# Performance work log

Measured on AMD Instinct MI355X. Metric: run time of the kernel, lower is better.

The kernel has to match this reference:

```python
import jax, jax.numpy as jnp
import numpy as np

HIDDEN = 4096
NH = 32        # num attention heads
NKV = 8        # num key/value heads
HD = 128       # q/k head dim
VHD = 96       # v head dim
ROT = 64       # rotary dim = int(HD * 0.5)
THETA = 10000.0
B, S = 2, 2048


def setup_inputs() -> dict:
    key = jax.random.key(0)
    ks = jax.random.split(key, 6)
    w = 0.02
    return {
        "hidden_states": jax.random.normal(ks[0], (B, S, HIDDEN), jnp.float32),
        "position_ids": jnp.arange(B * S, dtype=jnp.int32).reshape(B, S) % S,
        "Wq": jax.random.normal(ks[1], (NH * HD, HIDDEN), jnp.float32) * w,
        "Wk": jax.random.normal(ks[2], (NKV * HD, HIDDEN), jnp.float32) * w,
        "Wv": jax.random.normal(ks[3], (NKV * VHD, HIDDEN), jnp.float32) * w,
        "Wo": jax.random.normal(ks[4], (HIDDEN, NH * VHD), jnp.float32) * w,
    }


def _rotate_half(x):
    x1, x2 = x[..., : x.shape[-1] // 2], x[..., x.shape[-1] // 2 :]
    return jnp.concatenate((-x2, x1), axis=-1)


def reference(hidden_states, position_ids, Wq, Wk, Wv, Wo):
    b, s, _ = hidden_states.shape
    # QKV projections (torch Linear: y = x @ W^T)
    q = (hidden_states @ Wq.T).reshape(b, s, NH, HD).transpose(0, 2, 1, 3)   # [b,NH,s,HD]
    k = (hidden_states @ Wk.T).reshape(b, s, NKV, HD).transpose(0, 2, 1, 3)  # [b,NKV,s,HD]
    v = (hidden_states @ Wv.T).reshape(b, s, NKV, VHD).transpose(0, 2, 1, 3)  # [b,NKV,s,VHD]

    # rotary embedding over first ROT dims (partial RoPE)
    inv_freq = 1.0 / (THETA ** (jnp.arange(0, ROT, 2, dtype=jnp.float32) / ROT))  # [ROT/2]
    freqs = position_ids.astype(jnp.float32)[:, :, None] * inv_freq              # [b,s,ROT/2]
    emb = jnp.concatenate((freqs, freqs), axis=-1)                                # [b,s,ROT]
    cos = jnp.cos(emb)[:, None, :, :].astype(hidden_states.dtype)                 # [b,1,s,ROT]
    sin = jnp.sin(emb)[:, None, :, :].astype(hidden_states.dtype)

    q_rot, q_pass = q[..., :ROT], q[..., ROT:]
    k_rot, k_pass = k[..., :ROT], k[..., ROT:]
    q_rot = q_rot * cos + _rotate_half(q_rot) * sin
    k_rot = k_rot * cos + _rotate_half(k_rot) * sin
    q = jnp.concatenate((q_rot, q_pass), axis=-1)
    k = jnp.concatenate((k_rot, k_pass), axis=-1)

    # GQA: repeat_kv (repeat_interleave over head dim)
    n_rep = NH // NKV
    k = jnp.repeat(k, n_rep, axis=1)  # [b,NH,s,HD]
    v = jnp.repeat(v, n_rep, axis=1)  # [b,NH,s,VHD]

    scores = jnp.einsum("bhqd,bhkd->bhqk", q, k) / np.float32(np.sqrt(HD))
    # causal additive mask (attention_mask as built by the HF model)
    neg = jnp.finfo(jnp.float32).min
    causal = jnp.where(jnp.tril(jnp.ones((s, s), dtype=bool)), 0.0, neg)
    scores = scores + causal[None, None, :, :]

    attn = jax.nn.softmax(scores.astype(jnp.float32), axis=-1).astype(q.dtype)
    out = jnp.einsum("bhqk,bhkd->bhqd", attn, v)          # [b,NH,s,VHD]
    out = out.transpose(0, 2, 1, 3).reshape(b, s, NH * VHD)
    return out @ Wo.T                                      # [b,s,HIDDEN]
```

## Files before the change

kernel.cpp:

```cpp
#include <hip/hip_runtime.h>

typedef __attribute__((ext_vector_type(4))) float f32x4;
typedef __attribute__((ext_vector_type(8))) __bf16 bf16x8;
typedef __attribute__((ext_vector_type(8))) unsigned short u16x8;
typedef __attribute__((ext_vector_type(4))) unsigned short u16x4;
typedef __attribute__((ext_vector_type(4))) short s16x4;
typedef unsigned short ushort_t;

__device__ __forceinline__ unsigned short f2bf(float x) {
  unsigned u = __builtin_bit_cast(unsigned, x);
  u += 0x7fffu + ((u >> 16) & 1u);
  return (unsigned short)(u >> 16);
}
__device__ __forceinline__ float bf2f(unsigned short h) {
  unsigned u = ((unsigned)h) << 16;
  return __builtin_bit_cast(float, u);
}
__device__ __forceinline__ short f2bf_n(float x) {
  return __builtin_bit_cast(short, (__bf16)x);
}

__device__ __forceinline__ void gload_lds16(const void* g, void* l) {
  __builtin_amdgcn_global_load_lds(
      (const __attribute__((address_space(1))) unsigned int*)g,
      (__attribute__((address_space(3))) unsigned int*)l, 16, 0, 0);
}

__global__ __launch_bounds__(256) void k_f32_to_bf16(
    const float* __restrict__ src, ushort_t* __restrict__ dst, int n8) {
  int i = blockIdx.x * 256 + threadIdx.x;
  if (i >= n8) return;
  float4 a = ((const float4*)src)[i * 2 + 0];
  float4 b = ((const float4*)src)[i * 2 + 1];
  u16x8 o;
  o[0] = f2bf(a.x); o[1] = f2bf(a.y); o[2] = f2bf(a.z); o[3] = f2bf(a.w);
  o[4] = f2bf(b.x); o[5] = f2bf(b.y); o[6] = f2bf(b.z); o[7] = f2bf(b.w);
  ((u16x8*)dst)[i] = o;
}

__global__ __launch_bounds__(256) void k_rope(
    ushort_t* __restrict__ QKV, const int* __restrict__ pos_ids) {
  int idx = blockIdx.x * 256 + threadIdx.x;
  if (idx >= 4096 * 40 * 32) return;
  int d = idx & 31;
  int rem = idx >> 5;
  int hh = rem % 40;
  int tk = rem / 40;
  int pos = pos_ids[tk];
  float inv = exp2f(-(float)d * (13.287712379549449f / 32.0f));
  float ang = (float)pos * inv;
  float s, c;
  __sincosf(ang, &s, &c);
  int col = (hh < 32) ? (hh * 128 + d) : (4096 + (hh - 32) * 128 + d);
  ushort_t* p = QKV + (size_t)tk * 5888 + col;
  float x1 = bf2f(p[0]);
  float x2 = bf2f(p[32]);
  p[0]  = f2bf(x1 * c - x2 * s);
  p[32] = f2bf(x2 * c + x1 * s);
}

template <int OUT_BF16>
__global__ __launch_bounds__(256, 2) void k_gemm_bt(
    const ushort_t* __restrict__ A, const ushort_t* __restrict__ B,
    void* __restrict__ C, int K, int lda, int ldb, int ldc) {
  __shared__ ushort_t lA[128 * 64];
  __shared__ ushort_t lB[128 * 64];
  const int t = threadIdx.x;
  const int ln = t & 63, w = t >> 6;
  const int fr = ln & 15, fg = ln >> 4;
  const int m0 = blockIdx.x * 128, n0 = blockIdx.y * 128;
  const int wr = (w >> 1) * 64, wc = (w & 1) * 64;

  const int srow = t >> 3;
  const int scol = ((((t & 7) * 16) ^ ((srow & 7) << 4)) >> 1);
  const ushort_t* pA = A + (srow + m0) * lda + scol;
  const ushort_t* pB = B + (srow + n0) * ldb + scol;
  char* lAb = (char*)lA + (w << 10);
  char* lBb = (char*)lB + (w << 10);

  f32x4 acc[4][4] = {};

  for (int k0 = 0; k0 < K; k0 += 64) {
    __syncthreads();
#pragma unroll
    for (int i = 0; i < 4; ++i) {
      gload_lds16(pA + i * 32 * lda + k0, lAb + i * 4096);
      gload_lds16(pB + i * 32 * ldb + k0, lBb + i * 4096);
    }
    __syncthreads();
#pragma unroll
    for (int kh = 0; kh < 2; ++kh) {
      bf16x8 af[4], bfv[4];
#pragma unroll
      for (int m = 0; m < 4; ++m) {
        int row = wr + m * 16 + fr;
        af[m] = *(const bf16x8*)((const char*)lA + row * 128 +
                                 ((kh * 64 + fg * 16) ^ ((row & 7) << 4)));
      }
#pragma unroll
      for (int n = 0; n < 4; ++n) {
        int row = wc + n * 16 + fr;
        bfv[n] = *(const bf16x8*)((const char*)lB + row * 128 +
                                  ((kh * 64 + fg * 16) ^ ((row & 7) << 4)));
      }
#pragma unroll
      for (int m = 0; m < 4; ++m)
#pragma unroll
        for (int n = 0; n < 4; ++n)
          acc[m][n] = __builtin_amdgcn_mfma_f32_16x16x32_bf16(
              af[m], bfv[n], acc[m][n], 0, 0, 0);
    }
  }
#pragma unroll
  for (int m = 0; m < 4; ++m)
#pragma unroll
    for (int n = 0; n < 4; ++n) {
      int row = m0 + wr + m * 16 + fg * 4;
      int col = n0 + wc + n * 16 + fr;
#pragma unroll
      for (int j = 0; j < 4; ++j) {
        if (OUT_BF16)
          ((ushort_t*)C)[(size_t)(row + j) * ldc + col] = f2bf(acc[m][n][j]);
        else
          ((float*)C)[(size_t)(row + j) * ldc + col] = acc[m][n][j];
      }
    }
}

__global__ __launch_bounds__(256, 2) void k_attn(
    const ushort_t* __restrict__ QKV, ushort_t* __restrict__ O) {
  __shared__ ushort_t lK[64 * 128];
  __shared__ ushort_t lV[16 * 96 * 4];

  const int t = threadIdx.x, ln = t & 63, w = t >> 6;
  const int fr = ln & 15, fg = ln >> 4;
  const int h = blockIdx.y, b = blockIdx.z;
  const int qt = ((h >> 4) & 1) ? (15 - (int)blockIdx.x) : (int)blockIdx.x;
  const int hk = h >> 2;
  const int q0 = qt * 128 + w * 32;
  const int tb = b * 2048;

  bf16x8 qf[2][4];
#pragma unroll
  for (int rq = 0; rq < 2; ++rq)
#pragma unroll
    for (int kb = 0; kb < 4; ++kb)
      qf[rq][kb] = *(const bf16x8*)(QKV +
                    (size_t)(tb + q0 + rq * 16 + fr) * 5888 + h * 128 +
                    kb * 32 + fg * 8);

  f32x4 oacc[6][2] = {};
  float mreg[2] = {-1e30f, -1e30f};
  float lreg[2] = {0.f, 0.f};

  const int krow = t >> 4;
  const int kse = ((((t & 15) * 16) ^ (((t >> 4) & 7) << 4)) >> 1);
  const int k4s = t / 12, c8s = t % 12;

  const float sc = 0.088388347648318447f;
  const float l2e = 1.4426950408889634f;
  const float scl2e = sc * l2e;

  const int nkt = (qt + 1) * 2;
  for (int kt = 0; kt < nkt; ++kt) {
    const int kb0 = kt * 64;
    __syncthreads();
    {
      const ushort_t* pK =
          QKV + (size_t)(tb + kb0 + krow) * 5888 + 4096 + hk * 128 + kse;
#pragma unroll
      for (int i = 0; i < 4; ++i)
        gload_lds16(pK + (size_t)i * 16 * 5888,
                    (char*)lK + i * 4096 + (w << 10));
    }
    if (t < 192) {
      const ushort_t* pV =
          QKV + (size_t)(tb + kb0 + k4s * 4) * 5888 + 5120 + hk * 96 + c8s * 8;
      u16x8 vrow[4];
#pragma unroll
      for (int kr = 0; kr < 4; ++kr)
        vrow[kr] = *(const u16x8*)(pV + (size_t)kr * 5888);
#pragma unroll
      for (int i = 0; i < 8; ++i) {
        int cs = (c8s * 8 + i) ^ (k4s & 15);
        u16x4 q;
#pragma unroll
        for (int kr = 0; kr < 4; ++kr) q[kr] = vrow[kr][i];
        *(u16x4*)(&lV[(k4s * 96 + cs) * 4]) = q;
      }
    }
    __syncthreads();
    if (kb0 > q0 + 31) continue;
    f32x4 s[4][2] = {};
    __builtin_amdgcn_s_setprio(1);
#pragma unroll
    for (int cb = 0; cb < 4; ++cb) {
      const int kv = cb * 16 + fr;
      bf16x8 kf[4];
#pragma unroll
      for (int kb = 0; kb < 4; ++kb)
        kf[kb] = *(const bf16x8*)((const char*)lK + kv * 256 +
                                  ((kb * 64 + fg * 16) ^ ((kv & 7) << 4)));
#pragma unroll
      for (int rq = 0; rq < 2; ++rq)
#pragma unroll
        for (int kb = 0; kb < 4; ++kb)
          s[cb][rq] = __builtin_amdgcn_mfma_f32_16x16x32_bf16(
              kf[kb], qf[rq][kb], s[cb][rq], 0, 0, 0);
    }
    __builtin_amdgcn_s_setprio(0);
    if (kb0 + 63 > q0) {
#pragma unroll
      for (int rq = 0; rq < 2; ++rq) {
        const int qrel = q0 + rq * 16 + fr - kb0;
#pragma unroll
        for (int cb = 0; cb < 4; ++cb)
#pragma unroll
          for (int j = 0; j < 4; ++j)
            if (cb * 16 + fg * 4 + j > qrel) s[cb][rq][j] = -3.0e38f;
      }
    }
    float pmax[2];
#pragma unroll
    for (int rq = 0; rq < 2; ++rq) {
      f32x4 rm4 = s[0][rq];
#pragma unroll
      for (int cb = 1; cb < 4; ++cb)
#pragma unroll
        for (int j = 0; j < 4; ++j) rm4[j] = fmaxf(rm4[j], s[cb][rq][j]);
      float rm = fmaxf(fmaxf(rm4[0], rm4[1]), fmaxf(rm4[2], rm4[3]));
      rm = fmaxf(rm, __shfl_xor(rm, 16, 64));
      rm = fmaxf(rm, __shfl_xor(rm, 32, 64));
      pmax[rq] = rm * sc;
    }
    bool need = (pmax[0] > mreg[0] + 6.f) || (pmax[1] > mreg[1] + 6.f);
    if (__any(need)) {
#pragma unroll
      for (int rq = 0; rq < 2; ++rq) {
        float mnew = fmaxf(mreg[rq], pmax[rq]);
        float sf = exp2f((mreg[rq] - mnew) * l2e);
        mreg[rq] = mnew;
        lreg[rq] *= sf;
#pragma unroll
        for (int c6 = 0; c6 < 6; ++c6) oacc[c6][rq] *= sf;
      }
    }
    s16x4 pb[4][2];
#pragma unroll
    for (int rq = 0; rq < 2; ++rq) {
      const float mb = mreg[rq] * l2e;
      f32x4 ps4 = {};
#pragma unroll
      for (int cb = 0; cb < 4; ++cb) {
#pragma unroll
        for (int j = 0; j < 4; ++j) {
          float p = exp2f(fmaf(s[cb][rq][j], scl2e, -mb));
          s[cb][rq][j] = p;
          ps4[j] += p;
        }
      }
      float ps = (ps4[0] + ps4[1]) + (ps4[2] + ps4[3]);
      ps += __shfl_xor(ps, 16, 64);
      ps += __shfl_xor(ps, 32, 64);
      lreg[rq] += ps;
#pragma unroll
      for (int cb = 0; cb < 4; ++cb) {
        s16x4 v;
#pragma unroll
        for (int j = 0; j < 4; ++j) v[j] = f2bf_n(s[cb][rq][j]);
        pb[cb][rq] = v;
      }
    }
    __builtin_amdgcn_s_setprio(1);
#pragma unroll
    for (int cb = 0; cb < 4; ++cb) {
      const int k4 = cb * 4 + fg;
      s16x4 va[6];
#pragma unroll
      for (int c6 = 0; c6 < 6; ++c6)
        va[c6] = *(const s16x4*)(
            &lV[(k4 * 96 + (((c6 * 16 + fr) ^ (k4 & 15)))) * 4]);
#pragma unroll
      for (int c6 = 0; c6 < 6; ++c6)
#pragma unroll
        for (int rq = 0; rq < 2; ++rq)
          oacc[c6][rq] = __builtin_amdgcn_mfma_f32_16x16x16bf16_1k(
              va[c6], pb[cb][rq], oacc[c6][rq], 0, 0, 0);
    }
    __builtin_amdgcn_s_setprio(0);
  }
#pragma unroll
  for (int rq = 0; rq < 2; ++rq) {
    const float inv = 1.0f / lreg[rq];
    const size_t rowb = (size_t)(tb + q0 + rq * 16 + fr) * 3072 + h * 96;
#pragma unroll
    for (int c6 = 0; c6 < 6; ++c6) {
      u16x4 o;
#pragma unroll
      for (int j = 0; j < 4; ++j)
        o[j] = (unsigned short)f2bf_n(oacc[c6][rq][j] * inv);
      *(u16x4*)(&O[rowb + c6 * 16 + fg * 4]) = o;
    }
  }
}

extern "C" void kernel_launch(void* const* d_in, const int* in_sizes, int n_in,
                              void* d_out, int out_size, void* d_ws,
                              size_t ws_size, hipStream_t stream) {
  const float* X  = (const float*)d_in[0];
  const int*   pos = (const int*)d_in[1];
  const float* Wq = (const float*)d_in[2];
  const float* Wk = (const float*)d_in[3];
  const float* Wv = (const float*)d_in[4];
  const float* Wo = (const float*)d_in[5];
  float* out = (float*)d_out;

  ushort_t* Xb    = (ushort_t*)d_ws;
  ushort_t* Wob   = Xb + 16777216;
  ushort_t* QKV   = Wob + 12582912;
  ushort_t* AO    = QKV + 24117248;
  ushort_t* Wqkvb = (ushort_t*)d_out;

  k_f32_to_bf16<<<8192, 256, 0, stream>>>(X, Xb, 2097152);
  k_f32_to_bf16<<<8192, 256, 0, stream>>>(Wq, Wqkvb, 2097152);
  k_f32_to_bf16<<<2048, 256, 0, stream>>>(Wk, Wqkvb + 16777216, 524288);
  k_f32_to_bf16<<<1536, 256, 0, stream>>>(Wv, Wqkvb + 20971520, 393216);
  k_f32_to_bf16<<<6144, 256, 0, stream>>>(Wo, Wob, 1572864);

  k_gemm_bt<1><<<dim3(32, 46), 256, 0, stream>>>(Xb, Wqkvb, QKV, 4096, 4096,
                                                 4096, 5888);
  k_rope<<<20480, 256, 0, stream>>>(QKV, pos);
  k_attn<<<dim3(16, 32, 2), 256, 0, stream>>>(QKV, AO);
  k_gemm_bt<0><<<dim3(32, 32), 256, 0, stream>>>(AO, Wob, out, 3072, 3072,
                                                 3072, 4096);
}
```

Baseline: 514.8 us.

## Replace GEMM with 512-thread 128x256 tile kernel using triple-buffered LDS prefetch

Both projection GEMMs now run on a new kernel with 8 waves per block and a 128x256 output tile. It keeps three LDS stages so global-to-LDS loads for tile k+2 overlap compute on tile k, and waits with vmcnt-based barriers instead of two __syncthreads per iteration. MFMA sections are wrapped in s_setprio to favour matrix issue. The cost is 144KB of LDS per block, which limits residency to one block per CU and makes the launch-bounds occupancy hint of 2 unreachable. The larger N tile also means fewer blocks, so wave-count tail effects may change.

```diff
diff --git a/kernel.cpp b/kernel.cpp
--- a/kernel.cpp
+++ b/kernel.cpp
@@ -60,63 +60,118 @@
 }
 
 template <int OUT_BF16>
-__global__ __launch_bounds__(256, 2) void k_gemm_bt(
+__global__ __launch_bounds__(512, 2) void k_gemm8(
     const ushort_t* __restrict__ A, const ushort_t* __restrict__ B,
     void* __restrict__ C, int K, int lda, int ldb, int ldc) {
-  __shared__ ushort_t lA[128 * 64];
-  __shared__ ushort_t lB[128 * 64];
+  __shared__ ushort_t lds[3][(128 + 256) * 64];
   const int t = threadIdx.x;
-  const int ln = t & 63, w = t >> 6;
+  const int w = t >> 6, ln = t & 63;
   const int fr = ln & 15, fg = ln >> 4;
-  const int m0 = blockIdx.x * 128, n0 = blockIdx.y * 128;
-  const int wr = (w >> 1) * 64, wc = (w & 1) * 64;
+  const int wm = w >> 2, wn = w & 3;
+  const int m0 = blockIdx.x * 128, n0 = blockIdx.y * 256;
 
   const int srow = t >> 3;
-  const int scol = ((((t & 7) * 16) ^ ((srow & 7) << 4)) >> 1);
-  const ushort_t* pA = A + (srow + m0) * lda + scol;
-  const ushort_t* pB = B + (srow + n0) * ldb + scol;
-  char* lAb = (char*)lA + (w << 10);
-  char* lBb = (char*)lB + (w << 10);
+  const int scolb = ((t & 7) * 16) ^ ((srow & 7) << 4);
+  const ushort_t* pA = A + (size_t)(m0 + srow) * lda + (scolb >> 1);
+  const ushort_t* pB = B + (size_t)(n0 + srow) * ldb + (scolb >> 1);
 
   f32x4 acc[4][4] = {};
 
-  for (int k0 = 0; k0 < K; k0 += 64) {
-    __syncthreads();
-#pragma unroll
-    for (int i = 0; i < 4; ++i) {
-      gload_lds16(pA + i * 32 * lda + k0, lAb + i * 4096);
-      gload_lds16(pB + i * 32 * ldb + k0, lBb + i * 4096);
-    }
-    __syncthreads();
-#pragma unroll
-    for (int kh = 0; kh < 2; ++kh) {
-      bf16x8 af[4], bfv[4];
-#pragma unroll
-      for (int m = 0; m < 4; ++m) {
-        int row = wr + m * 16 + fr;
-        af[m] = *(const bf16x8*)((const char*)lA + row * 128 +
-                                 ((kh * 64 + fg * 16) ^ ((row & 7) << 4)));
-      }
-#pragma unroll
-      for (int n = 0; n < 4; ++n) {
-        int row = wc + n * 16 + fr;
-        bfv[n] = *(const bf16x8*)((const char*)lB + row * 128 +
-                                  ((kh * 64 + fg * 16) ^ ((row & 7) << 4)));
-      }
+  const int nt = K >> 6;
+
+#define STAGE(bufi, k0)                                                       \
+  {                                                                           \
+    char* d_ = (char*)&lds[(bufi)][0];                                        \
+    _Pragma("unroll") for (int i_ = 0; i_ < 2; ++i_)                          \
+        gload_lds16(pA + (size_t)i_ * 64 * lda + (k0),                        \
+                    d_ + i_ * 8192 + t * 16);                                 \
+    char* dB_ = d_ + 16384;                                                   \
+    _Pragma("unroll") for (int i_ = 0; i_ < 4; ++i_)                          \
+        gload_lds16(pB + (size_t)i_ * 64 * ldb + (k0),                        \
+                    dB_ + i_ * 8192 + t * 16);                                \
+  }
+
+  STAGE(0, 0)
+  STAGE(1, 64)
+  asm volatile("s_waitcnt vmcnt(6)" ::: "memory");
+  __builtin_amdgcn_s_barrier();
+  asm volatile("" ::: "memory");
+
+  for (int kt = 0; kt < nt; ++kt) {
+    const int cur = kt % 3;
+    if (kt + 2 < nt) STAGE((kt + 2) % 3, (kt + 2) << 6)
+    const char* bA = (const char*)&lds[cur][0];
+    const char* bB = bA + 16384;
+
+    bf16x8 af[4][2];
+#pragma unroll
+    for (int m = 0; m < 4; ++m) {
+      const int r = wm * 64 + m * 16 + fr;
+#pragma unroll
+      for (int kk = 0; kk < 2; ++kk)
+        af[m][kk] = *(const bf16x8*)(bA + r * 128 +
+                                     ((kk * 64 + fg * 16) ^ ((r & 7) << 4)));
+    }
+    {
+      bf16x8 bfv[2][2];
+#pragma unroll
+      for (int n = 0; n < 2; ++n) {
+        const int r = wn * 64 + n * 16 + fr;
+#pragma unroll
+        for (int kk = 0; kk < 2; ++kk)
+          bfv[n][kk] = *(const bf16x8*)(bB + r * 128 +
+                                        ((kk * 64 + fg * 16) ^ ((r & 7) << 4)));
+      }
+      __builtin_amdgcn_s_setprio(1);
 #pragma unroll
       for (int m = 0; m < 4; ++m)
 #pragma unroll
-        for (int n = 0; n < 4; ++n)
-          acc[m][n] = __builtin_amdgcn_mfma_f32_16x16x32_bf16(
-              af[m], bfv[n], acc[m][n], 0, 0, 0);
+        for (int n = 0; n < 2; ++n)
+#pragma unroll
+          for (int kk = 0; kk < 2; ++kk)
+            acc[m][n] = __builtin_amdgcn_mfma_f32_16x16x32_bf16(
+                af[m][kk], bfv[n][kk], acc[m][n], 0, 0, 0);
+      __builtin_amdgcn_s_setprio(0);
+    }
+    {
+      bf16x8 bfv[2][2];
+#pragma unroll
+      for (int n = 0; n < 2; ++n) {
+        const int r = wn * 64 + (n + 2) * 16 + fr;
+#pragma unroll
+        for (int kk = 0; kk < 2; ++kk)
+          bfv[n][kk] = *(const bf16x8*)(bB + r * 128 +
+                                        ((kk * 64 + fg * 16) ^ ((r & 7) << 4)));
+      }
+      __builtin_amdgcn_s_setprio(1);
+#pragma unroll
+      for (int m = 0; m < 4; ++m)
+#pragma unroll
+        for (int n = 0; n < 2; ++n)
+#pragma unroll
+          for (int kk = 0; kk < 2; ++kk)
+            acc[m][n + 2] = __builtin_amdgcn_mfma_f32_16x16x32_bf16(
+                af[m][kk], bfv[n][kk], acc[m][n + 2], 0, 0, 0);
+      __builtin_amdgcn_s_setprio(0);
+    }
+    if (kt + 1 < nt) {
+      __builtin_amdgcn_sched_barrier(0);
+      if (kt + 2 < nt)
+        asm volatile("s_waitcnt vmcnt(6)" ::: "memory");
+      else
+        asm volatile("s_waitcnt vmcnt(0)" ::: "memory");
+      __builtin_amdgcn_s_barrier();
+      asm volatile("" ::: "memory");
     }
   }
+#undef STAGE
+
 #pragma unroll
   for (int m = 0; m < 4; ++m)
 #pragma unroll
     for (int n = 0; n < 4; ++n) {
-      int row = m0 + wr + m * 16 + fg * 4;
-      int col = n0 + wc + n * 16 + fr;
+      const int row = m0 + wm * 64 + m * 16 + fg * 4;
+      const int col = n0 + wn * 64 + n * 16 + fr;
 #pragma unroll
       for (int j = 0; j < 4; ++j) {
         if (OUT_BF16)
@@ -327,10 +382,10 @@
   k_f32_to_bf16<<<1536, 256, 0, stream>>>(Wv, Wqkvb + 20971520, 393216);
   k_f32_to_bf16<<<6144, 256, 0, stream>>>(Wo, Wob, 1572864);
 
-  k_gemm_bt<1><<<dim3(32, 46), 256, 0, stream>>>(Xb, Wqkvb, QKV, 4096, 4096,
-                                                 4096, 5888);
+  k_gemm8<1><<<dim3(32, 23), 512, 0, stream>>>(Xb, Wqkvb, QKV, 4096, 4096,
+                                               4096, 5888);
   k_rope<<<20480, 256, 0, stream>>>(QKV, pos);
   k_attn<<<dim3(16, 32, 2), 256, 0, stream>>>(QKV, AO);
-  k_gemm_bt<0><<<dim3(32, 32), 256, 0, stream>>>(AO, Wob, out, 3072, 3072,
-                                                 3072, 4096);
-}
+  k_gemm8<0><<<dim3(32, 16), 512, 0, stream>>>(AO, Wob, out, 3072, 3072,
+                                               3072, 4096);
+}
```

New measurement: 517.5 us. Within noise of the previous version (+0.5%).
